# Kernel tuning notes

Measured on AMD Instinct MI355X. Metric: run time of the kernel, lower is better.

The kernel has to match this reference:

```python
import jax, jax.numpy as jnp
import numpy as np

MARGIN = 0.3
EPS = 1e-6      # torch F.pairwise_distance eps used inside TripletMarginLoss
BIG = 1000000.0  # same sentinel as original code


def setup_inputs() -> dict:
    key = jax.random.key(0)
    k1, k2 = jax.random.split(key)
    embeddings = jax.random.normal(k1, (4096, 2048), dtype=jnp.float32)
    labels = jax.random.randint(k2, (4096,), 0, 128)  # 128 identities -> ~32 samples each
    return {"embeddings": embeddings, "labels": labels}


def _batch_hard_triplet_loss(emb, labels):
    B = emb.shape[0]
    # pairwise euclidean distances (torch.cdist p=2)
    sq = jnp.sum(emb * emb, axis=1)                      # [B]
    d2 = sq[:, None] + sq[None, :] - 2.0 * (emb @ emb.T)  # [B,B]
    dists = jnp.sqrt(jnp.maximum(d2, 0.0))

    same = labels[:, None] == labels[None, :]            # [B,B] bool
    eye = jnp.eye(B, dtype=bool)
    pos_mask = same & ~eye

    # hard positive: argmax over same-label (self set to -1, others-with-diff-label masked to 0*d -> use -1 uniformly for non-positives, matching dists*mask_pos with diag=-1 since dists>=0)
    pos_d = jnp.where(pos_mask, dists, -1.0)
    hard_pos = jnp.argmax(pos_d, axis=1)                 # [B]
    # hard negative: argmin over different-label (same-label gets +1e6 like original)
    neg_d = jnp.where(same, dists + BIG, dists)
    hard_neg = jnp.argmin(neg_d, axis=1)                 # [B]

    # valid anchors: at least one positive (other than self) and one negative
    valid = (jnp.sum(pos_mask, axis=1) > 0) & (jnp.sum(~same, axis=1) > 0)

    # TripletMarginLoss recomputes distances with eps added to the difference
    dp = jnp.linalg.norm(emb - emb[hard_pos] + EPS, axis=1)
    dn = jnp.linalg.norm(emb - emb[hard_neg] + EPS, axis=1)
    per = jnp.maximum(dp - dn + MARGIN, 0.0)

    cnt = jnp.sum(valid)
    total = jnp.sum(jnp.where(valid, per, 0.0))
    return jnp.where(cnt > 0, total / jnp.maximum(cnt, 1).astype(per.dtype), 0.0)


def reference(embeddings, labels):
    return _batch_hard_triplet_loss(embeddings, labels)
```

## Files before the change

### kernel.cpp

```cpp
#include <hip/hip_runtime.h>
#include <stdint.h>

#define B 4096
#define D 2048
#define BK 128
#define NITER (D / BK)
#define BM 64
#define BN 128

typedef unsigned long long ull;
typedef float f32x4 __attribute__((ext_vector_type(4)));
typedef long v2l __attribute__((ext_vector_type(2)));

#define SENT_P 0x00000000FFFFFFFFull
#define SENT_N (~0ull)

__device__ __forceinline__ void async_copy16(const unsigned char* g, unsigned char* l) {
  __builtin_amdgcn_global_load_lds(
      (const __attribute__((address_space(1))) unsigned int*)g,
      (__attribute__((address_space(3))) unsigned int*)l,
      16, 0, 0);
}

__global__ void k_convert_sq(const float* __restrict__ emb,
                             unsigned char* __restrict__ embq,
                             float* __restrict__ sq,
                             float* __restrict__ rs,
                             ull* __restrict__ bp,
                             ull* __restrict__ bn,
                             float* __restrict__ red_sum,
                             int* __restrict__ red_cnt,
                             int* __restrict__ red_done) {
  const int row = blockIdx.x, t = threadIdx.x;
  const float4* src = (const float4*)(emb + (size_t)row * D);
  float4 v0 = src[2 * t], v1 = src[2 * t + 1];
  float s = v0.x * v0.x + v0.y * v0.y + v0.z * v0.z + v0.w * v0.w
          + v1.x * v1.x + v1.y * v1.y + v1.z * v1.z + v1.w * v1.w;
  float sm = v0.x + v0.y + v0.z + v0.w + v1.x + v1.y + v1.z + v1.w;

  unsigned w0 = __builtin_amdgcn_cvt_pk_fp8_f32(v0.x, v0.y, 0, false);
  w0 = __builtin_amdgcn_cvt_pk_fp8_f32(v0.z, v0.w, w0, true);
  unsigned w1 = __builtin_amdgcn_cvt_pk_fp8_f32(v1.x, v1.y, 0, false);
  w1 = __builtin_amdgcn_cvt_pk_fp8_f32(v1.z, v1.w, w1, true);
  uint2 o; o.x = w0; o.y = w1;
  const int pos = ((t >> 4) << 7) | ((t & 3) << 5) | (((t >> 2) & 3) << 3);
  *(uint2*)(embq + (size_t)row * D + pos) = o;

  for (int off = 32; off; off >>= 1) {
    s  += __shfl_down(s, off, 64);
    sm += __shfl_down(sm, off, 64);
  }
  __shared__ float ps[4], pm[4];
  int lane = t & 63, wave = t >> 6;
  if (lane == 0) { ps[wave] = s; pm[wave] = sm; }
  __syncthreads();
  if (t == 0) {
    sq[row] = ps[0] + ps[1] + ps[2] + ps[3];
    rs[row] = pm[0] + pm[1] + pm[2] + pm[3];
    bp[row] = SENT_P;
    bn[row] = SENT_N;
    if (row == 0) { *red_sum = 0.0f; *red_cnt = 0; *red_done = 0; }
  }
}

__launch_bounds__(256, 3)
__global__ void k_gemm_select(const unsigned char* __restrict__ embq,
                              const float* __restrict__ sq,
                              const int* __restrict__ labels,
                              ull* __restrict__ best_pos,
                              ull* __restrict__ best_neg) {
  __shared__ __align__(16) unsigned char ldsA[2][BM * BK];
  __shared__ __align__(16) unsigned char ldsB[2][BN * BK];

  int rem = blockIdx.x, p = 0;
  while (rem >= 2 * (32 - p)) { rem -= 2 * (32 - p); ++p; }
  int by = 2 * p;
  int c = 32 - p;
  if (rem >= c) { by += 1; rem -= c; }
  const int bx = p + rem;

  const int tid  = threadIdx.x;
  const int lane = tid & 63;
  const int wave = tid >> 6;
  const int wm = wave >> 1, wn = wave & 1;
  const int q = lane >> 4, m15 = lane & 15;
  const int ibase = by * BM, jbase = bx * BN;

  int aoff[2][2], boff[2][4];
#pragma unroll
  for (int sh = 0; sh < 2; ++sh) {
#pragma unroll
    for (int g = 0; g < 2; ++g) {
      int ra = wm * 32 + g * 16 + m15;
      aoff[sh][g] = ra * BK + (((q * 2 + sh) ^ (ra & 7)) * 16);
    }
#pragma unroll
    for (int g = 0; g < 4; ++g) {
      int rb = wn * 64 + g * 16 + m15;
      boff[sh][g] = rb * BK + (((q * 2 + sh) ^ (rb & 7)) * 16);
    }
  }

  const int srow = lane >> 3;
  const int slot = lane & 7;
  size_t agoff[2], bgoff[4];
  int lasta[2], lastb[4];
#pragma unroll
  for (int pp = 0; pp < 2; ++pp) {
    int r0  = wave * 16 + pp * 8;
    int row = r0 + srow;
    agoff[pp] = (size_t)(ibase + row) * D + (slot ^ (row & 7)) * 16;
    lasta[pp] = r0 * BK;
  }
#pragma unroll
  for (int pp = 0; pp < 4; ++pp) {
    int r0  = wave * 32 + pp * 8;
    int row = r0 + srow;
    bgoff[pp] = (size_t)(jbase + row) * D + (slot ^ (row & 7)) * 16;
    lastb[pp] = r0 * BK;
  }

  f32x4 acc[2][4];
  const f32x4 z = {0.f, 0.f, 0.f, 0.f};
#pragma unroll
  for (int a = 0; a < 2; ++a)
#pragma unroll
    for (int b = 0; b < 4; ++b) acc[a][b] = z;

  auto stage = [&](int buf, int kb) {
#pragma unroll
    for (int pp = 0; pp < 2; ++pp)
      async_copy16(embq + agoff[pp] + kb, &ldsA[buf][lasta[pp]]);
#pragma unroll
    for (int pp = 0; pp < 4; ++pp)
      async_copy16(embq + bgoff[pp] + kb, &ldsB[buf][lastb[pp]]);
  };

  auto compute = [&](int buf) {
#pragma unroll
    for (int sh = 0; sh < 2; ++sh) {
      v2l af[2], bf[4];
#pragma unroll
      for (int g = 0; g < 2; ++g) af[g] = *(const v2l*)&ldsA[buf][aoff[sh][g]];
#pragma unroll
      for (int g = 0; g < 4; ++g) bf[g] = *(const v2l*)&ldsB[buf][boff[sh][g]];
#pragma unroll
      for (int mi = 0; mi < 2; ++mi)
#pragma unroll
        for (int ni = 0; ni < 4; ++ni)
          acc[mi][ni] = __builtin_amdgcn_mfma_f32_16x16x32_fp8_fp8(
              af[mi][0], bf[ni][0], acc[mi][ni], 0, 0, 0);
#pragma unroll
      for (int mi = 0; mi < 2; ++mi)
#pragma unroll
        for (int ni = 0; ni < 4; ++ni)
          acc[mi][ni] = __builtin_amdgcn_mfma_f32_16x16x32_fp8_fp8(
              af[mi][1], bf[ni][1], acc[mi][ni], 0, 0, 0);
    }
  };

  stage(0, 0);
  asm volatile("s_waitcnt vmcnt(0)" ::: "memory");
  __builtin_amdgcn_s_barrier();
  asm volatile("" ::: "memory");

  for (int t = 0; t < NITER; ++t) {
    if (t + 1 < NITER) stage((t + 1) & 1, (t + 1) * BK);
    compute(t & 1);
    asm volatile("s_waitcnt vmcnt(0)" ::: "memory");
    __builtin_amdgcn_s_barrier();
    asm volatile("" ::: "memory");
  }

  float sqj[4];
  int labj[4];
#pragma unroll
  for (int ni = 0; ni < 4; ++ni) {
    int jj = jbase + wn * 64 + ni * 16 + m15;
    sqj[ni] = sq[jj];
    labj[ni] = labels[jj];
  }

  ull colBp[4], colBn[4];
#pragma unroll
  for (int ni = 0; ni < 4; ++ni) { colBp[ni] = SENT_P; colBn[ni] = SENT_N; }

#pragma unroll
  for (int mi = 0; mi < 2; ++mi) {
#pragma unroll
    for (int r = 0; r < 4; ++r) {
      const int i = ibase + wm * 32 + mi * 16 + q * 4 + r;
      const float si = sq[i];
      const int li = labels[i];
      ull bp = SENT_P;
      ull bn = SENT_N;
#pragma unroll
      for (int ni = 0; ni < 4; ++ni) {
        int jj = jbase + wn * 64 + ni * 16 + m15;
        if (jj > i) {
          float dot = acc[mi][ni][r];
          float d2 = si + sqj[ni] - 2.0f * dot;
          float dist = sqrtf(fmaxf(d2, 0.0f));
          ull pv = ((ull)__float_as_uint(dist)) << 32;
          if (labj[ni] == li) {
            ull cr = pv | (unsigned)(~jj);
            bp = bp > cr ? bp : cr;
            ull cc = pv | (unsigned)(~i);
            colBp[ni] = colBp[ni] > cc ? colBp[ni] : cc;
          } else {
            ull cr = pv | (unsigned)jj;
            bn = bn < cr ? bn : cr;
            ull cc = pv | (unsigned)i;
            colBn[ni] = colBn[ni] < cc ? colBn[ni] : cc;
          }
        }
      }
#pragma unroll
      for (int off = 1; off <= 8; off <<= 1) {
        ull op = __shfl_xor(bp, off, 64);
        ull on = __shfl_xor(bn, off, 64);
        bp = bp > op ? bp : op;
        bn = bn < on ? bn : on;
      }
      if (m15 == 0) {
        if (bp != SENT_P) atomicMax(&best_pos[i], bp);
        if (bn != SENT_N) atomicMin(&best_neg[i], bn);
      }
    }
  }

#pragma unroll
  for (int ni = 0; ni < 4; ++ni) {
    ull cp = colBp[ni], cn = colBn[ni];
#pragma unroll
    for (int off = 16; off <= 32; off <<= 1) {
      ull op = __shfl_xor(cp, off, 64);
      ull on = __shfl_xor(cn, off, 64);
      cp = cp > op ? cp : op;
      cn = cn < on ? cn : on;
    }
    if (q == 0) {
      int j = jbase + wn * 64 + ni * 16 + m15;
      if (cp != SENT_P) atomicMax(&best_pos[j], cp);
      if (cn != SENT_N) atomicMin(&best_neg[j], cn);
    }
  }
}

__global__ void k_loss_final(const ull* __restrict__ best_pos,
                             const ull* __restrict__ best_neg,
                             const float* __restrict__ rs,
                             float* __restrict__ red_sum,
                             int* __restrict__ red_cnt,
                             int* __restrict__ red_done,
                             float* __restrict__ out) {
  const int i = blockIdx.x * 256 + threadIdx.x;
  float per = 0.0f;
  int v = 0;
  ull bp = best_pos[i], bn = best_neg[i];
  if (bp != SENT_P && bn != SENT_N) {
    unsigned pRaw = ~(unsigned)bp;
    unsigned nRaw = (unsigned)bn;
    int pi = pRaw < (unsigned)B ? (int)pRaw : 0;
    int ni = nRaw < (unsigned)B ? (int)nRaw : 0;
    float distp = __uint_as_float((unsigned)(bp >> 32));
    float distn = __uint_as_float((unsigned)(bn >> 32));
    float ri = rs[i];
    const float e = 1e-6f, de2 = (float)D * 1e-12f;
    float dp2 = distp * distp + 2.0f * e * (ri - rs[pi]) + de2;
    float dn2 = distn * distn + 2.0f * e * (ri - rs[ni]) + de2;
    float dp = sqrtf(fmaxf(dp2, 0.0f));
    float dn = sqrtf(fmaxf(dn2, 0.0f));
    per = fmaxf(dp - dn + 0.3f, 0.0f);
    v = 1;
  }
  for (int off = 32; off; off >>= 1) {
    per += __shfl_down(per, off, 64);
    v   += __shfl_down(v, off, 64);
  }
  __shared__ float pps[4];
  __shared__ int pvs[4];
  int lane = threadIdx.x & 63, wave = threadIdx.x >> 6;
  if (lane == 0) { pps[wave] = per; pvs[wave] = v; }
  __syncthreads();
  if (threadIdx.x == 0) {
    float t = pps[0] + pps[1] + pps[2] + pps[3];
    int cv = pvs[0] + pvs[1] + pvs[2] + pvs[3];
    atomicAdd(red_sum, t);
    atomicAdd(red_cnt, cv);
    __threadfence();
    int old = atomicAdd(red_done, 1);
    if (old == (int)gridDim.x - 1) {
      float s = atomicAdd(red_sum, 0.0f);
      int cc = atomicAdd(red_cnt, 0);
      out[0] = cc > 0 ? s / (float)cc : 0.0f;
    }
  }
}

extern "C" void kernel_launch(void* const* d_in, const int* in_sizes, int n_in,
                              void* d_out, int out_size, void* d_ws, size_t ws_size,
                              hipStream_t stream) {
  const float* emb = (const float*)d_in[0];
  const int* labels = (const int*)d_in[1];
  float* out = (float*)d_out;
  char* ws = (char*)d_ws;

  const size_t off_embq = 0;
  const size_t off_sq   = off_embq + (size_t)B * D;
  const size_t off_rs   = off_sq + (size_t)B * 4;
  const size_t off_bp   = off_rs + (size_t)B * 4;
  const size_t off_bn   = off_bp + (size_t)B * 8;
  const size_t off_red  = off_bn + (size_t)B * 8;

  unsigned char* embq = (unsigned char*)(ws + off_embq);
  float* sq   = (float*)(ws + off_sq);
  float* rs   = (float*)(ws + off_rs);
  ull* bp     = (ull*)(ws + off_bp);
  ull* bn     = (ull*)(ws + off_bn);
  float* red_sum = (float*)(ws + off_red);
  int* red_cnt   = (int*)(ws + off_red + 4);
  int* red_done  = (int*)(ws + off_red + 8);

  hipLaunchKernelGGL(k_convert_sq, dim3(B), dim3(256), 0, stream,
                     emb, embq, sq, rs, bp, bn, red_sum, red_cnt, red_done);
  hipLaunchKernelGGL(k_gemm_select, dim3(1056), dim3(256), 0, stream,
                     embq, sq, labels, bp, bn);
  hipLaunchKernelGGL(k_loss_final, dim3(B / 256), dim3(256), 0, stream,
                     bp, bn, rs, red_sum, red_cnt, red_done, out);
}
```

Measured before the change: 135.6 us.

## Use scaled 16x16x128 FP8 MFMA and single-buffer LDS for higher occupancy

Replaces the pairs of 16x16x32 FP8 MFMAs with a single scaled 16x16x128 f8f6f4 MFMA per tile, using unit scales (0x7F exponent), so the instruction count for the GEMM drops by four times. The LDS double buffer is collapsed to a single buffer with plain __syncthreads around each load, and launch bounds are raised to 4 blocks per CU. The aim is higher matrix-core throughput and occupancy, at the cost of no longer overlapping the next tile's global-to-LDS copy with compute inside a block. The K-fragment ordering must match how the 128-wide instruction expects operands, or results could differ.

```diff
diff --git a/kernel.cpp b/kernel.cpp
--- a/kernel.cpp
+++ b/kernel.cpp
@@ -11,6 +11,7 @@
 typedef unsigned long long ull;
 typedef float f32x4 __attribute__((ext_vector_type(4)));
 typedef long v2l __attribute__((ext_vector_type(2)));
+typedef int i32x8 __attribute__((ext_vector_type(8)));
 
 #define SENT_P 0x00000000FFFFFFFFull
 #define SENT_N (~0ull)
@@ -63,14 +64,14 @@
   }
 }
 
-__launch_bounds__(256, 3)
+__launch_bounds__(256, 4)
 __global__ void k_gemm_select(const unsigned char* __restrict__ embq,
                               const float* __restrict__ sq,
                               const int* __restrict__ labels,
                               ull* __restrict__ best_pos,
                               ull* __restrict__ best_neg) {
-  __shared__ __align__(16) unsigned char ldsA[2][BM * BK];
-  __shared__ __align__(16) unsigned char ldsB[2][BN * BK];
+  __shared__ __align__(16) unsigned char ldsA[BM * BK];
+  __shared__ __align__(16) unsigned char ldsB[BN * BK];
 
   int rem = blockIdx.x, p = 0;
   while (rem >= 2 * (32 - p)) { rem -= 2 * (32 - p); ++p; }
@@ -127,49 +128,38 @@
 #pragma unroll
     for (int b = 0; b < 4; ++b) acc[a][b] = z;
 
-  auto stage = [&](int buf, int kb) {
+  union fragu { v2l h[2]; i32x8 w; };
+
+  for (int kb = 0; kb < D; kb += BK) {
+    __syncthreads();
 #pragma unroll
     for (int pp = 0; pp < 2; ++pp)
-      async_copy16(embq + agoff[pp] + kb, &ldsA[buf][lasta[pp]]);
+      async_copy16(embq + agoff[pp] + kb, &ldsA[lasta[pp]]);
 #pragma unroll
     for (int pp = 0; pp < 4; ++pp)
-      async_copy16(embq + bgoff[pp] + kb, &ldsB[buf][lastb[pp]]);
-  };
-
-  auto compute = [&](int buf) {
-#pragma unroll
-    for (int sh = 0; sh < 2; ++sh) {
-      v2l af[2], bf[4];
-#pragma unroll
-      for (int g = 0; g < 2; ++g) af[g] = *(const v2l*)&ldsA[buf][aoff[sh][g]];
-#pragma unroll
-      for (int g = 0; g < 4; ++g) bf[g] = *(const v2l*)&ldsB[buf][boff[sh][g]];
-#pragma unroll
-      for (int mi = 0; mi < 2; ++mi)
-#pragma unroll
-        for (int ni = 0; ni < 4; ++ni)
-          acc[mi][ni] = __builtin_amdgcn_mfma_f32_16x16x32_fp8_fp8(
-              af[mi][0], bf[ni][0], acc[mi][ni], 0, 0, 0);
-#pragma unroll
-      for (int mi = 0; mi < 2; ++mi)
-#pragma unroll
-        for (int ni = 0; ni < 4; ++ni)
-          acc[mi][ni] = __builtin_amdgcn_mfma_f32_16x16x32_fp8_fp8(
-              af[mi][1], bf[ni][1], acc[mi][ni], 0, 0, 0);
-    }
-  };
-
-  stage(0, 0);
-  asm volatile("s_waitcnt vmcnt(0)" ::: "memory");
-  __builtin_amdgcn_s_barrier();
-  asm volatile("" ::: "memory");
-
-  for (int t = 0; t < NITER; ++t) {
-    if (t + 1 < NITER) stage((t + 1) & 1, (t + 1) * BK);
-    compute(t & 1);
-    asm volatile("s_waitcnt vmcnt(0)" ::: "memory");
-    __builtin_amdgcn_s_barrier();
-    asm volatile("" ::: "memory");
+      async_copy16(embq + bgoff[pp] + kb, &ldsB[lastb[pp]]);
+    __syncthreads();
+
+    fragu fa[2], fb[4];
+#pragma unroll
+    for (int g = 0; g < 2; ++g) {
+      fa[g].h[0] = *(const v2l*)&ldsA[aoff[0][g]];
+      fa[g].h[1] = *(const v2l*)&ldsA[aoff[1][g]];
+    }
+#pragma unroll
+    for (int ni = 0; ni < 4; ++ni) {
+      fb[ni].h[0] = *(const v2l*)&ldsB[boff[0][ni]];
+      fb[ni].h[1] = *(const v2l*)&ldsB[boff[1][ni]];
+    }
+#pragma unroll
+    for (int mi = 0; mi < 2; ++mi)
+#pragma unroll
+      for (int ni = 0; ni < 4; ++ni)
+        acc[mi][ni] = __builtin_amdgcn_mfma_scale_f32_16x16x128_f8f6f4(
+            fa[mi].w, fb[ni].w, acc[mi][ni],
+            0 , 0 ,
+            0, 0x7F7F7F7Fu ,
+            0, 0x7F7F7F7Fu );
   }
 
   float sqj[4];
```

Result: slower. 252.6 us (+86.2%).
